# Performance work log

Hardware: AMD Instinct MI355X
Metric: run time of the kernel (lower is better)

Reference implementation:

```python
import jax, jax.numpy as jnp
import numpy as np

B, N = 2, 2048
TOP_K = 48
NUM_RBF = 16
MAX_REL = 32            # max_relative_feature
NUM_POS = 16            # num_positional_embeddings
EDGE_FEATURES = 128
EDGE_IN = NUM_POS + NUM_RBF * 25  # 416
POS_IN = 2 * MAX_REL + 2          # 66 one-hot classes


def setup_inputs() -> dict:
    key = jax.random.key(0)
    k0, k1, k2, k3 = jax.random.split(key, 4)
    X = jax.random.normal(k0, (B, N, 4, 3), dtype=jnp.float32) * 3.0
    mask = jnp.ones((B, N), dtype=jnp.float32)
    R_idx = jnp.arange(B * N, dtype=jnp.int32).reshape(B, N)
    chain_labels = jax.random.randint(k1, (B, N), 0, 4).astype(jnp.int32)
    W_pos = 0.05 * jax.random.normal(k2, (POS_IN, NUM_POS), dtype=jnp.float32)
    b_pos = jnp.zeros((NUM_POS,), dtype=jnp.float32)
    W_edge = 0.05 * jax.random.normal(k3, (EDGE_IN, EDGE_FEATURES), dtype=jnp.float32)
    b_edge = jnp.zeros((EDGE_FEATURES,), dtype=jnp.float32)
    return {"X": X, "mask": mask, "R_idx": R_idx, "chain_labels": chain_labels,
            "W_pos": W_pos, "b_pos": b_pos, "W_edge": W_edge, "b_edge": b_edge}


def _rbf(D):
    # D: [..., K] -> [..., K, NUM_RBF]
    mu = jnp.linspace(2.0, 22.0, NUM_RBF)        # D_min=2, D_max=22
    sigma = (22.0 - 2.0) / NUM_RBF               # 1.25
    return jnp.exp(-(((D[..., None] - mu) / sigma) ** 2))


def _pair_dist(A, Bc):
    # A, Bc: [B, N, 3] -> [B, N, N]
    return jnp.sqrt(jnp.sum((A[:, :, None, :] - Bc[:, None, :, :]) ** 2, axis=-1) + 1e-6)


def reference(X, mask, R_idx, chain_labels, W_pos, b_pos, W_edge, b_edge):
    # virtual Cbeta from backbone geometry
    b = X[:, :, 1, :] - X[:, :, 0, :]
    c = X[:, :, 2, :] - X[:, :, 1, :]
    a = jnp.cross(b, c, axis=-1)
    Cb = -0.58273431 * a + 0.56802827 * b - 0.54067466 * c + X[:, :, 1, :]
    Ca, Nat, Cat, Oat = X[:, :, 1, :], X[:, :, 0, :], X[:, :, 2, :], X[:, :, 3, :]

    # masked Ca-Ca distances + k nearest neighbors
    mask2 = mask[:, None, :] * mask[:, :, None]
    D = mask2 * _pair_dist(Ca, Ca)
    D_adjust = D + (1.0 - mask2) * jnp.max(D, axis=-1, keepdims=True)
    neg_D, E_idx = jax.lax.top_k(-D_adjust, min(TOP_K, N))  # smallest distances
    D_neighbors = -neg_D                                     # [B, N, K]

    rbfs = [_rbf(D_neighbors)]
    pairs = [(Nat, Nat), (Cat, Cat), (Oat, Oat), (Cb, Cb),
             (Ca, Nat), (Ca, Cat), (Ca, Oat), (Ca, Cb),
             (Nat, Cat), (Nat, Oat), (Nat, Cb), (Cb, Cat), (Cb, Oat), (Oat, Cat),
             (Nat, Ca), (Cat, Ca), (Oat, Ca), (Cb, Ca),
             (Cat, Nat), (Oat, Nat), (Cb, Nat), (Cat, Cb), (Oat, Cb), (Cat, Oat)]
    for A_, B_ in pairs:  # fixed structural set of 24 atom-pair types
        Dab = _pair_dist(A_, B_)                          # [B, N, N]
        Dn = jnp.take_along_axis(Dab, E_idx, axis=2)      # [B, N, K]
        rbfs.append(_rbf(Dn))
    RBF_all = jnp.concatenate(rbfs, axis=-1)              # [B, N, K, 25*NUM_RBF]

    # relative positional / chain features at the gathered neighbors
    offset = R_idx[:, :, None] - R_idx[:, None, :]
    offset = jnp.take_along_axis(offset, E_idx, axis=2)   # [B, N, K]
    d_chains = (chain_labels[:, :, None] == chain_labels[:, None, :]).astype(jnp.int32)
    E_chains = jnp.take_along_axis(d_chains, E_idx, axis=2)

    d = jnp.clip(offset + MAX_REL, 0, 2 * MAX_REL)
    d = d * E_chains + (1 - E_chains) * (2 * MAX_REL + 1)
    d_onehot = jax.nn.one_hot(d, POS_IN, dtype=jnp.float32)  # [B, N, K, 66]
    E_positional = d_onehot @ W_pos + b_pos                  # [B, N, K, 16]

    E = jnp.concatenate((E_positional, RBF_all), axis=-1)    # [B, N, K, 416]
    E = E @ W_edge + b_edge                                  # [B, N, K, 128]
    return E, E_idx
```

## Files before the change

kernel.cpp:

```cpp
#include <hip/hip_runtime.h>
#include <hip/hip_bf16.h>
#include <stdint.h>

#define BB   2
#define NN   2048
#define BN   (BB*NN)
#define KTOP 48
#define EIN  416
#define EF   128

typedef __attribute__((ext_vector_type(8))) short s8v;
typedef __attribute__((ext_vector_type(4))) float f32x4;
typedef __attribute__((ext_vector_type(4))) unsigned int u32x4;
typedef unsigned short u16;
typedef unsigned int u32;
typedef unsigned long long u64;

__device__ __constant__ int cPA[25] = {1,0,2,3,4,1,1,1,1,0,0,0,4,4,3,0,2,3,4,2,3,4,2,3,2};
__device__ __constant__ int cPB[25] = {1,0,2,3,4,0,2,3,4,2,3,4,2,3,2,1,1,1,1,0,0,0,4,4,3};

__device__ __forceinline__ u16 bf16u(float x) {
  __hip_bfloat16 h = __float2bfloat16(x);
  return *reinterpret_cast<u16*>(&h);
}
__device__ __forceinline__ u32 pack2(float lo, float hi) {
  return (u32)bf16u(lo) | ((u32)bf16u(hi) << 16);
}
__device__ __forceinline__ u32 cvtpk(float lo, float hi) {
  u32 r;
  asm("v_cvt_pk_bf16_f32 %0, %1, %2" : "=v"(r) : "v"(lo), "v"(hi));
  return r;
}

__global__ __launch_bounds__(256) void prep_kernel(const float* __restrict__ X,
                                                   const float* __restrict__ W_edge,
                                                   float* __restrict__ atoms5p,
                                                   float* __restrict__ capack4,
                                                   u16* __restrict__ wtf) {
  int tid = blockIdx.x * 256 + threadIdx.x;
  if (tid < EIN * EF) {
    int k = tid >> 7, n = tid & 127;
    wtf[((size_t)(k >> 3)) * 1024 + n * 8 + (k & 7)] = bf16u(W_edge[tid]);
  } else if (tid < EIN * EF + BN) {
    int idx = tid - EIN * EF;
    const float* x = X + (size_t)idx * 12;
    float Nx = x[0], Ny = x[1], Nz = x[2];
    float Cax = x[3], Cay = x[4], Caz = x[5];
    float Cx = x[6], Cy = x[7], Cz = x[8];
    float Ox = x[9], Oy = x[10], Oz = x[11];
    float bx = Cax - Nx, by = Cay - Ny, bz = Caz - Nz;
    float cx = Cx - Cax, cy = Cy - Cay, cz = Cz - Caz;
    float ax = by * cz - bz * cy;
    float ay = bz * cx - bx * cz;
    float az = bx * cy - by * cx;
    float Cbx = -0.58273431f * ax + 0.56802827f * bx - 0.54067466f * cx + Cax;
    float Cby = -0.58273431f * ay + 0.56802827f * by - 0.54067466f * cy + Cay;
    float Cbz = -0.58273431f * az + 0.56802827f * bz - 0.54067466f * cz + Caz;
    f32x4* o = (f32x4*)(atoms5p + (size_t)idx * 20);
    o[0] = (f32x4){Nx, Ny, Nz, 0.f};
    o[1] = (f32x4){Cax, Cay, Caz, 0.f};
    o[2] = (f32x4){Cx, Cy, Cz, 0.f};
    o[3] = (f32x4){Ox, Oy, Oz, 0.f};
    o[4] = (f32x4){Cbx, Cby, Cbz, 0.f};
    *(f32x4*)(capack4 + (size_t)idx * 4) = (f32x4){Cax, Cay, Caz, 0.f};
  }
}

__device__ __forceinline__ u32 blockExclScan(u32 v, u32* scanw, int t) {
  int lane = t & 63, w = t >> 6;
  u32 inc = v;
#pragma unroll
  for (int off = 1; off < 64; off <<= 1) {
    u32 o = __shfl_up(inc, off);
    if (lane >= off) inc += o;
  }
  if (lane == 63) scanw[w] = inc;
  __syncthreads();
  u32 base = 0;
  for (int ww = 0; ww < w; ++ww) base += scanw[ww];
  __syncthreads();
  return base + inc - v;
}

template<int NB, bool CHKPREF>
__device__ __forceinline__ void radix_round(u32* hist, u32* scanw, u32* selinfo, int t,
                                            const u32* kv, u32 pref, int prefShift,
                                            int binShift, u32 binMask, u32 r) {
  const int PB = NB / 256;
#pragma unroll
  for (int q = 0; q < PB / 4; ++q)
    *(u32x4*)&hist[t * PB + q * 4] = (u32x4){0, 0, 0, 0};
  __syncthreads();
#pragma unroll
  for (int s = 0; s < 8; ++s) {
    bool ok = (!CHKPREF) || ((kv[s] >> prefShift) == pref);
    if (ok) atomicAdd(&hist[(kv[s] >> binShift) & binMask], 1u);
  }
  __syncthreads();
  u32 loc[PB];
  u32 sum = 0;
#pragma unroll
  for (int q = 0; q < PB / 4; ++q) {
    u32x4 lv = *(u32x4*)&hist[t * PB + q * 4];
    loc[q * 4 + 0] = lv.x; loc[q * 4 + 1] = lv.y;
    loc[q * 4 + 2] = lv.z; loc[q * 4 + 3] = lv.w;
    sum += lv.x + lv.y + lv.z + lv.w;
  }
  int lane = t & 63, w = t >> 6;
  u32 inc = sum;
#pragma unroll
  for (int off = 1; off < 64; off <<= 1) {
    u32 o = __shfl_up(inc, off);
    if (lane >= off) inc += o;
  }
  if (lane == 63) scanw[w] = inc;
  __syncthreads();
  u32 base = 0;
  for (int ww = 0; ww < w; ++ww) base += scanw[ww];
  u32 c = base + inc - sum;
#pragma unroll
  for (int q = 0; q < PB; ++q) {
    u32 nc = c + loc[q];
    if (c < r && r <= nc) { selinfo[0] = (u32)(t * PB + q); selinfo[1] = r - c; }
    c = nc;
  }
  __syncthreads();
}

__global__ __launch_bounds__(256) void topk_kernel(const float* __restrict__ capack4,
                                                   const float* __restrict__ mask,
                                                   float* __restrict__ dtop,
                                                   float* __restrict__ eidx_f) {
  __shared__ u32 hist[4096];
  __shared__ u32 scanw[4];
  __shared__ u32 selinfo[2];
  __shared__ float redf[4];
  __shared__ u64 win[64];

  int row = blockIdx.x;
  int b = row >> 11, i = row & (NN - 1);
  int t = threadIdx.x, lane = t & 63, w = t >> 6;
  const float* cab4 = capack4 + (size_t)b * NN * 4;
  const float* mrow = mask + (size_t)b * NN;
  f32x4 ci = *(const f32x4*)&cab4[(size_t)i * 4];
  float mi = mrow[i];
  f32x4 mk0 = *(const f32x4*)&mrow[t * 8];
  f32x4 mk1 = *(const f32x4*)&mrow[t * 8 + 4];

  float dvv[8], m2v[8];
  float lmax = 0.f;
#pragma unroll
  for (int s = 0; s < 8; ++s) {
    f32x4 cj = *(const f32x4*)&cab4[(size_t)(t * 8 + s) * 4];
    float dx = ci.x - cj.x, dy = ci.y - cj.y, dz = ci.z - cj.z;
    float d = sqrtf(dx * dx + dy * dy + dz * dz + 1e-6f);
    float mj = (s < 4) ? mk0[s] : mk1[s - 4];
    float m2 = mi * mj;
    float D = m2 * d;
    dvv[s] = D; m2v[s] = m2;
    lmax = fmaxf(lmax, D);
  }
#pragma unroll
  for (int off = 32; off >= 1; off >>= 1) lmax = fmaxf(lmax, __shfl_xor(lmax, off));
  if (lane == 0) redf[w] = lmax;
  __syncthreads();
  float rmax = fmaxf(fmaxf(redf[0], redf[1]), fmaxf(redf[2], redf[3]));

  u32 kv[8];
#pragma unroll
  for (int s = 0; s < 8; ++s)
    kv[s] = __float_as_uint(dvv[s] + (1.0f - m2v[s]) * rmax);

  u32 r = KTOP;
  radix_round<4096, false>(hist, scanw, selinfo, t, kv, 0, 0, 20, 0xFFFu, r);
  u32 sel1 = selinfo[0]; r = selinfo[1];
  radix_round<1024, true>(hist, scanw, selinfo, t, kv, sel1, 20, 10, 0x3FFu, r);
  u32 sel2 = selinfo[0]; r = selinfo[1];
  u32 pref12 = (sel1 << 10) | sel2;
  radix_round<1024, true>(hist, scanw, selinfo, t, kv, pref12, 10, 0, 0x3FFu, r);
  u32 sel3 = selinfo[0];
  u32 takeEq = selinfo[1];
  u32 T = (sel1 << 20) | (sel2 << 10) | sel3;

  u32 lcnt = 0, ecnt = 0;
#pragma unroll
  for (int s = 0; s < 8; ++s) { lcnt += (kv[s] < T); ecnt += (kv[s] == T); }
  u32 ebase = blockExclScan(ecnt, scanw, t);
  u32 taken = 0;
  if (ebase < takeEq) { u32 room = takeEq - ebase; taken = room < ecnt ? room : ecnt; }
  u32 wbase = blockExclScan(lcnt + taken, scanw, t);
  u32 slot = wbase, tleft = taken;
#pragma unroll
  for (int s = 0; s < 8; ++s) {
    u32 j = (u32)(t * 8 + s);
    if (kv[s] < T) {
      win[slot++] = ((u64)kv[s] << 32) | j;
    } else if (kv[s] == T && tleft) {
      win[slot++] = ((u64)kv[s] << 32) | j;
      tleft--;
    }
  }
  __syncthreads();

  if (w == 0) {
    u64 key = (lane < KTOP) ? win[lane] : ~0ull;
#pragma unroll
    for (int k = 2; k <= 64; k <<= 1) {
#pragma unroll
      for (int jj = k >> 1; jj >= 1; jj >>= 1) {
        u64 p = __shfl_xor(key, jj);
        bool lowerl = (lane & jj) == 0;
        bool asc = (lane & k) == 0;
        u64 mn = p < key ? p : key;
        u64 mx = p < key ? key : p;
        key = (lowerl == asc) ? mn : mx;
      }
    }
    if (lane < KTOP) {
      u32 j = (u32)(key & 0xffffffffu);
      eidx_f[row * KTOP + lane] = (float)j;
      dtop[row * KTOP + lane] = __uint_as_float((u32)(key >> 32));
    }
  }
}

__device__ __forceinline__ s8v rbf8(float D, float mu0) {
  float Dc = fminf(D, 40.0f);
  float t0 = (Dc - mu0) * 0.8f;
  float v0 = __expf(-t0 * t0);
  float g = __expf(fmaf(2.13333333f, t0, -1.13777778f));
  const float C = 0.10273985f;
  float v1 = v0 * g; g *= C;
  float v2 = v1 * g; g *= C;
  float v3 = v2 * g; g *= C;
  float v4 = v3 * g; g *= C;
  float v5 = v4 * g; g *= C;
  float v6 = v5 * g; g *= C;
  float v7 = v6 * g;
  union { u32x4 u; s8v s; } cv;
  cv.u = (u32x4){cvtpk(v0, v1), cvtpk(v2, v3), cvtpk(v4, v5), cvtpk(v6, v7)};
  return cv.s;
}

__global__ __launch_bounds__(64) void edge_kernel(const float* __restrict__ atoms5p,
                                                  const u16* __restrict__ wtf,
                                                  const float* __restrict__ eidx_f,
                                                  const float* __restrict__ dtop,
                                                  const int* __restrict__ Ridx,
                                                  const int* __restrict__ chains,
                                                  const float* __restrict__ Wpos,
                                                  const float* __restrict__ bpos,
                                                  const float* __restrict__ bedge,
                                                  float* __restrict__ Eout) {
  __shared__ float D_lds[KTOP][26];
  __shared__ u32 pos_lds[KTOP][8];
  __shared__ int jbuf[KTOP];
  __shared__ f32x4 aI_lds[5];

  int lane = threadIdx.x;
  int row = blockIdx.x;
  int b = row >> 11, i = row & (NN - 1);
  const float* atomsB = atoms5p + (size_t)b * NN * 20;

  if (lane < 5) aI_lds[lane] = *(const f32x4*)&atomsB[(size_t)i * 20 + lane * 4];
  if (lane < KTOP) {
    int j = (int)eidx_f[(size_t)row * KTOP + lane];
    jbuf[lane] = j;
    D_lds[lane][0] = dtop[(size_t)row * KTOP + lane];
    int Ri = Ridx[b * NN + i], Rj = Ridx[b * NN + j];
    int same = (chains[b * NN + i] == chains[b * NN + j]);
    int off = Ri - Rj + 32;
    off = off < 0 ? 0 : (off > 64 ? 64 : off);
    int drow = same ? off : 65;
    const float* wr = Wpos + drow * 16;
    u32 pk[8];
#pragma unroll
    for (int h = 0; h < 4; ++h) {
      f32x4 wv = *(const f32x4*)&wr[h * 4];
      f32x4 bv = *(const f32x4*)&bpos[h * 4];
      pk[h * 2 + 0] = cvtpk(wv.x + bv.x, wv.y + bv.y);
      pk[h * 2 + 1] = cvtpk(wv.z + bv.z, wv.w + bv.w);
    }
    *(u32x4*)&pos_lds[lane][0] = (u32x4){pk[0], pk[1], pk[2], pk[3]};
    *(u32x4*)&pos_lds[lane][4] = (u32x4){pk[4], pk[5], pk[6], pk[7]};
  }

#pragma unroll
  for (int q = 0; q < 18; ++q) {
    int e = q * 64 + lane;
    int k = e / 24;
    int p = e - k * 24 + 1;
    int j = jbuf[k];
    f32x4 I = aI_lds[cPA[p]];
    f32x4 J = *(const f32x4*)&atomsB[(size_t)j * 20 + cPB[p] * 4];
    float dx = I.x - J.x, dy = I.y - J.y, dz = I.z - J.z;
    D_lds[k][p] = __builtin_amdgcn_sqrtf(dx * dx + dy * dy + dz * dz + 1e-6f);
  }

  int lr = lane & 15, lg = lane >> 4;
  const u16* wk = wtf + (size_t)lg * 1024 + lr * 8;
  const float MU8 = 12.6666667f;
  f32x4 acc[3][8] = {};

  {
    s8v a0, a1, a2;
    if (lg < 2) {
      a0 = *reinterpret_cast<const s8v*>(&pos_lds[lr][lg * 4]);
      a1 = *reinterpret_cast<const s8v*>(&pos_lds[16 + lr][lg * 4]);
      a2 = *reinterpret_cast<const s8v*>(&pos_lds[32 + lr][lg * 4]);
    } else {
      float mu0 = (lg == 2) ? 2.0f : MU8;
      a0 = rbf8(D_lds[lr][0], mu0);
      a1 = rbf8(D_lds[16 + lr][0], mu0);
      a2 = rbf8(D_lds[32 + lr][0], mu0);
    }
#pragma unroll
    for (int nt = 0; nt < 8; ++nt) {
      s8v bv = *reinterpret_cast<const s8v*>(wk + nt * 128);
      acc[0][nt] = __builtin_amdgcn_mfma_f32_16x16x32_bf16(a0, bv, acc[0][nt], 0, 0, 0);
      acc[1][nt] = __builtin_amdgcn_mfma_f32_16x16x32_bf16(a1, bv, acc[1][nt], 0, 0, 0);
      acc[2][nt] = __builtin_amdgcn_mfma_f32_16x16x32_bf16(a2, bv, acc[2][nt], 0, 0, 0);
    }
  }
#pragma unroll
  for (int kc = 1; kc < 13; ++kc) {
    int p = 2 * kc - 1 + (lg >> 1);
    float mu0 = (lg & 1) ? MU8 : 2.0f;
    s8v a0 = rbf8(D_lds[lr][p], mu0);
    s8v a1 = rbf8(D_lds[16 + lr][p], mu0);
    s8v a2 = rbf8(D_lds[32 + lr][p], mu0);
    const u16* wkc = wk + (size_t)kc * 4096;
#pragma unroll
    for (int nt = 0; nt < 8; ++nt) {
      s8v bv = *reinterpret_cast<const s8v*>(wkc + nt * 128);
      acc[0][nt] = __builtin_amdgcn_mfma_f32_16x16x32_bf16(a0, bv, acc[0][nt], 0, 0, 0);
      acc[1][nt] = __builtin_amdgcn_mfma_f32_16x16x32_bf16(a1, bv, acc[1][nt], 0, 0, 0);
      acc[2][nt] = __builtin_amdgcn_mfma_f32_16x16x32_bf16(a2, bv, acc[2][nt], 0, 0, 0);
    }
  }

  float bias[8];
#pragma unroll
  for (int nt = 0; nt < 8; ++nt) bias[nt] = bedge[nt * 16 + lr];
  float* orow = Eout + (size_t)row * KTOP * EF;
#pragma unroll
  for (int mt = 0; mt < 3; ++mt) {
#pragma unroll
    for (int qq = 0; qq < 4; ++qq) {
      float* pr = orow + (size_t)(mt * 16 + lg * 4 + qq) * EF + lr;
#pragma unroll
      for (int nt = 0; nt < 8; ++nt)
        pr[nt * 16] = acc[mt][nt][qq] + bias[nt];
    }
  }
}

extern "C" void kernel_launch(void* const* d_in, const int* in_sizes, int n_in,
                              void* d_out, int out_size, void* d_ws, size_t ws_size,
                              hipStream_t stream) {
  const float* X = (const float*)d_in[0];
  const float* mask = (const float*)d_in[1];
  const int* Ridx = (const int*)d_in[2];
  const int* chains = (const int*)d_in[3];
  const float* Wpos = (const float*)d_in[4];
  const float* bpos = (const float*)d_in[5];
  const float* Wedge = (const float*)d_in[6];
  const float* bedge = (const float*)d_in[7];

  float* Eout = (float*)d_out;
  float* EidxF = Eout + (size_t)BN * KTOP * EF;

  u16* wtf = (u16*)d_ws;
  float* atoms5p = (float*)((char*)d_ws + 53248 * 2);
  float* capack4 = atoms5p + (size_t)BN * 20;
  float* dtop = capack4 + (size_t)BN * 4;

  prep_kernel<<<(EIN * EF + BN + 255) / 256, 256, 0, stream>>>(X, Wedge, atoms5p, capack4, wtf);
  topk_kernel<<<BN, 256, 0, stream>>>(capack4, mask, dtop, EidxF);
  edge_kernel<<<BN, 64, 0, stream>>>(atoms5p, wtf, EidxF, dtop, Ridx, chains, Wpos, bpos, bedge, Eout);
}
```

Baseline: 92.72 us.

## Split edge kernel into three blocks per row, one per 16-neighbor tile

The edge kernel now launches three single-wave blocks per residue row, each handling 16 of the 48 neighbors instead of all of them. Accumulators shrink from 24 to 8 MFMA tiles per wave, and launch bounds ask for 5 waves per SIMD, aiming for higher occupancy and more blocks to hide latency. In exchange, each block reloads the full W_edge bf16 fragments and the central atom data, so weight traffic through cache triples. The dead pack2 helper is removed.

```diff
diff --git a/kernel.cpp b/kernel.cpp
--- a/kernel.cpp
+++ b/kernel.cpp
@@ -22,9 +22,6 @@
 __device__ __forceinline__ u16 bf16u(float x) {
   __hip_bfloat16 h = __float2bfloat16(x);
   return *reinterpret_cast<u16*>(&h);
-}
-__device__ __forceinline__ u32 pack2(float lo, float hi) {
-  return (u32)bf16u(lo) | ((u32)bf16u(hi) << 16);
 }
 __device__ __forceinline__ u32 cvtpk(float lo, float hi) {
   u32 r;
@@ -242,31 +239,34 @@
   return cv.s;
 }
 
-__global__ __launch_bounds__(64) void edge_kernel(const float* __restrict__ atoms5p,
-                                                  const u16* __restrict__ wtf,
-                                                  const float* __restrict__ eidx_f,
-                                                  const float* __restrict__ dtop,
-                                                  const int* __restrict__ Ridx,
-                                                  const int* __restrict__ chains,
-                                                  const float* __restrict__ Wpos,
-                                                  const float* __restrict__ bpos,
-                                                  const float* __restrict__ bedge,
-                                                  float* __restrict__ Eout) {
-  __shared__ float D_lds[KTOP][26];
-  __shared__ u32 pos_lds[KTOP][8];
-  __shared__ int jbuf[KTOP];
+__global__ __launch_bounds__(64, 5) void edge_kernel(const float* __restrict__ atoms5p,
+                                                     const u16* __restrict__ wtf,
+                                                     const float* __restrict__ eidx_f,
+                                                     const float* __restrict__ dtop,
+                                                     const int* __restrict__ Ridx,
+                                                     const int* __restrict__ chains,
+                                                     const float* __restrict__ Wpos,
+                                                     const float* __restrict__ bpos,
+                                                     const float* __restrict__ bedge,
+                                                     float* __restrict__ Eout) {
+  __shared__ float D_lds[16][26];
+  __shared__ u32 pos_lds[16][8];
+  __shared__ int jbuf[16];
   __shared__ f32x4 aI_lds[5];
 
   int lane = threadIdx.x;
-  int row = blockIdx.x;
+  int bid = blockIdx.x;
+  int row = bid / 3, mt = bid - row * 3;
   int b = row >> 11, i = row & (NN - 1);
+  int kbase = mt * 16;
   const float* atomsB = atoms5p + (size_t)b * NN * 20;
 
   if (lane < 5) aI_lds[lane] = *(const f32x4*)&atomsB[(size_t)i * 20 + lane * 4];
-  if (lane < KTOP) {
-    int j = (int)eidx_f[(size_t)row * KTOP + lane];
+  if (lane < 16) {
+    int k = kbase + lane;
+    int j = (int)eidx_f[(size_t)row * KTOP + k];
     jbuf[lane] = j;
-    D_lds[lane][0] = dtop[(size_t)row * KTOP + lane];
+    D_lds[lane][0] = dtop[(size_t)row * KTOP + k];
     int Ri = Ridx[b * NN + i], Rj = Ridx[b * NN + j];
     int same = (chains[b * NN + i] == chains[b * NN + j]);
     int off = Ri - Rj + 32;
@@ -286,72 +286,58 @@
   }
 
 #pragma unroll
-  for (int q = 0; q < 18; ++q) {
+  for (int q = 0; q < 6; ++q) {
     int e = q * 64 + lane;
-    int k = e / 24;
-    int p = e - k * 24 + 1;
-    int j = jbuf[k];
+    int kl = e / 24;
+    int p = e - kl * 24 + 1;
+    int j = jbuf[kl];
     f32x4 I = aI_lds[cPA[p]];
     f32x4 J = *(const f32x4*)&atomsB[(size_t)j * 20 + cPB[p] * 4];
     float dx = I.x - J.x, dy = I.y - J.y, dz = I.z - J.z;
-    D_lds[k][p] = __builtin_amdgcn_sqrtf(dx * dx + dy * dy + dz * dz + 1e-6f);
+    D_lds[kl][p] = __builtin_amdgcn_sqrtf(dx * dx + dy * dy + dz * dz + 1e-6f);
   }
 
   int lr = lane & 15, lg = lane >> 4;
   const u16* wk = wtf + (size_t)lg * 1024 + lr * 8;
   const float MU8 = 12.6666667f;
-  f32x4 acc[3][8] = {};
+  f32x4 acc[8] = {};
 
   {
-    s8v a0, a1, a2;
+    s8v af;
     if (lg < 2) {
-      a0 = *reinterpret_cast<const s8v*>(&pos_lds[lr][lg * 4]);
-      a1 = *reinterpret_cast<const s8v*>(&pos_lds[16 + lr][lg * 4]);
-      a2 = *reinterpret_cast<const s8v*>(&pos_lds[32 + lr][lg * 4]);
+      af = *reinterpret_cast<const s8v*>(&pos_lds[lr][lg * 4]);
     } else {
-      float mu0 = (lg == 2) ? 2.0f : MU8;
-      a0 = rbf8(D_lds[lr][0], mu0);
-      a1 = rbf8(D_lds[16 + lr][0], mu0);
-      a2 = rbf8(D_lds[32 + lr][0], mu0);
+      af = rbf8(D_lds[lr][0], (lg == 2) ? 2.0f : MU8);
     }
 #pragma unroll
     for (int nt = 0; nt < 8; ++nt) {
       s8v bv = *reinterpret_cast<const s8v*>(wk + nt * 128);
-      acc[0][nt] = __builtin_amdgcn_mfma_f32_16x16x32_bf16(a0, bv, acc[0][nt], 0, 0, 0);
-      acc[1][nt] = __builtin_amdgcn_mfma_f32_16x16x32_bf16(a1, bv, acc[1][nt], 0, 0, 0);
-      acc[2][nt] = __builtin_amdgcn_mfma_f32_16x16x32_bf16(a2, bv, acc[2][nt], 0, 0, 0);
+      acc[nt] = __builtin_amdgcn_mfma_f32_16x16x32_bf16(af, bv, acc[nt], 0, 0, 0);
     }
   }
 #pragma unroll
   for (int kc = 1; kc < 13; ++kc) {
     int p = 2 * kc - 1 + (lg >> 1);
     float mu0 = (lg & 1) ? MU8 : 2.0f;
-    s8v a0 = rbf8(D_lds[lr][p], mu0);
-    s8v a1 = rbf8(D_lds[16 + lr][p], mu0);
-    s8v a2 = rbf8(D_lds[32 + lr][p], mu0);
+    s8v af = rbf8(D_lds[lr][p], mu0);
     const u16* wkc = wk + (size_t)kc * 4096;
 #pragma unroll
     for (int nt = 0; nt < 8; ++nt) {
       s8v bv = *reinterpret_cast<const s8v*>(wkc + nt * 128);
-      acc[0][nt] = __builtin_amdgcn_mfma_f32_16x16x32_bf16(a0, bv, acc[0][nt], 0, 0, 0);
-      acc[1][nt] = __builtin_amdgcn_mfma_f32_16x16x32_bf16(a1, bv, acc[1][nt], 0, 0, 0);
-      acc[2][nt] = __builtin_amdgcn_mfma_f32_16x16x32_bf16(a2, bv, acc[2][nt], 0, 0, 0);
+      acc[nt] = __builtin_amdgcn_mfma_f32_16x16x32_bf16(af, bv, acc[nt], 0, 0, 0);
     }
   }
 
   float bias[8];
 #pragma unroll
   for (int nt = 0; nt < 8; ++nt) bias[nt] = bedge[nt * 16 + lr];
-  float* orow = Eout + (size_t)row * KTOP * EF;
-#pragma unroll
-  for (int mt = 0; mt < 3; ++mt) {
-#pragma unroll
-    for (int qq = 0; qq < 4; ++qq) {
-      float* pr = orow + (size_t)(mt * 16 + lg * 4 + qq) * EF + lr;
-#pragma unroll
-      for (int nt = 0; nt < 8; ++nt)
-        pr[nt * 16] = acc[mt][nt][qq] + bias[nt];
-    }
+  float* orow = Eout + ((size_t)row * KTOP + kbase) * EF;
+#pragma unroll
+  for (int qq = 0; qq < 4; ++qq) {
+    float* pr = orow + (size_t)(lg * 4 + qq) * EF + lr;
+#pragma unroll
+    for (int nt = 0; nt < 8; ++nt)
+      pr[nt * 16] = acc[nt][qq] + bias[nt];
   }
 }
 
@@ -377,5 +363,5 @@
 
   prep_kernel<<<(EIN * EF + BN + 255) / 256, 256, 0, stream>>>(X, Wedge, atoms5p, capack4, wtf);
   topk_kernel<<<BN, 256, 0, stream>>>(capack4, mask, dtop, EidxF);
-  edge_kernel<<<BN, 64, 0, stream>>>(atoms5p, wtf, EidxF, dtop, Ridx, chains, Wpos, bpos, bedge, Eout);
-}
+  edge_kernel<<<BN * 3, 64, 0, stream>>>(atoms5p, wtf, EidxF, dtop, Ridx, chains, Wpos, bpos, bedge, Eout);
+}
```

After: 95.65 us. 1.03x slower.
